# Optimization experiments

Measured on AMD Instinct MI355X. Metric: run time of the kernel, lower is better.

The kernel has to match this reference:

```python
import jax, jax.numpy as jnp
import numpy as np

N, E, B = 100000, 800000, 64
IN, HC1, HC2, NC, SA = 256, 128, 32, 2, 350
NEG = 0.2  # GATv2Conv default negative_slope


def forward(s_x, s_edge_index, s_batch, s_root_n_id,
            Wq, bq, Wk, bk, Wv, bv,
            Wl1, bl1, Wr1, br1, att1, bias1,
            Wl2, bl2, Wr2, br2, att2, bias2,
            Wl3, bl3, Wr3, br3, att3, bias3,
            c1w, c1b, c2W, c2b, c3W, c3b,
            linW, linb, aW1, ab1, aW2, mW1, mb1, mW2, mb2):
    src, dst = s_edge_index[0], s_edge_index[1]
    x_info = s_x
    # --- SelfAttention over seq_len=1 (x.unsqueeze(1)) ---
    z = s_x[:, None, :]                                   # [N,1,IN]
    q = z @ Wq + bq; k = z @ Wk + bk; v = z @ Wv + bv      # [N,1,SA]
    scores = jnp.einsum('nqd,nkd->nqk', q, k) / jnp.sqrt(jnp.float32(SA))
    probs = jax.nn.softmax(scores, axis=-1)
    h = jnp.einsum('nqk,nkd->nqd', probs, v)[:, 0, :]      # [N,SA]

    def gatv2(x, Wl, bl, Wr, br, att, bias):
        # PyG GATv2Conv, heads=1, eval mode (dropout off)
        xl = x @ Wl + bl                                   # source transform [N,O]
        xr = x @ Wr + br                                   # target transform [N,O]
        e = jax.nn.leaky_relu(xl[src] + xr[dst], NEG)      # [E,O]
        s = e @ att                                        # [E]
        smax = jax.ops.segment_max(s, dst, num_segments=N)
        smax = jnp.where(jnp.isfinite(smax), smax, 0.0)
        ex = jnp.exp(s - smax[dst])
        den = jax.ops.segment_sum(ex, dst, num_segments=N)
        alpha = ex / jnp.maximum(den[dst], 1e-16)
        return jax.ops.segment_sum(alpha[:, None] * xl[src], dst, num_segments=N) + bias

    h = jax.nn.relu(gatv2(h, Wl1, bl1, Wr1, br1, att1, bias1))
    h = jax.nn.relu(gatv2(h, Wl2, bl2, Wr2, br2, att2, bias2))
    h = jax.nn.relu(gatv2(h, Wl3, bl3, Wr3, br3, att3, bias3))   # [N,HC2]

    # --- readout: root node feature ++ global mean pool ---
    cnt = jax.ops.segment_sum(jnp.ones((N,), h.dtype), s_batch, num_segments=B)
    pooled = jax.ops.segment_sum(h, s_batch, num_segments=B) / jnp.maximum(cnt, 1.0)[:, None]
    sx = jnp.concatenate([h[s_root_n_id], pooled], axis=-1)       # [B,2*HC2]

    # --- info branch on raw root features ---
    info = x_info[s_root_n_id]                                    # [B,IN]
    info = c1w[0] * info[:, :-2] + c1w[1] * info[:, 1:-1] + c1w[2] * info[:, 2:] + c1b  # Conv1d(1,1,3)
    t = info.T                                                    # [IN-2,B]
    t = jax.nn.relu(c2W @ t + c2b[:, None])                       # [HC1,B]
    t = jax.nn.relu(c3W @ t + c3b[:, None])                       # [HC1//2,B]
    t = t.T                                                       # [B,HC1//2]
    L = t.shape[1]
    t = jax.nn.relu(t.reshape(B, HC2, L // HC2).mean(-1))         # AdaptiveAvgPool1d(HC2)

    sx = jax.nn.relu(sx @ linW + linb)                            # [B,HC2]

    # --- semantic attention over the two views ---
    emb = jnp.stack([sx, t], axis=1)                              # [B,2,HC2]
    w = jnp.tanh(emb @ aW1 + ab1) @ aW2                           # [B,2,1]
    beta = jax.nn.softmax(w, axis=1)
    emb = (beta * emb).sum(1)                                     # [B,HC2]

    return jax.nn.softmax(jnp.tanh(emb @ mW1 + mb1) @ mW2 + mb2, axis=1)  # [B,NC]


def setup_inputs() -> dict:
    keys = iter(jax.random.split(jax.random.key(0), 64))
    def nrm(*shape):
        return jax.random.normal(next(keys), shape, dtype=jnp.float32) * 0.05
    inp = {}
    inp['s_x'] = jax.random.normal(next(keys), (N, IN), dtype=jnp.float32)
    inp['s_edge_index'] = jax.random.randint(next(keys), (2, E), 0, N)
    inp['s_batch'] = jnp.sort(jax.random.randint(next(keys), (N,), 0, B))
    inp['s_root_n_id'] = jax.random.randint(next(keys), (B,), 0, N)
    inp['Wq'] = nrm(IN, SA); inp['bq'] = nrm(SA)
    inp['Wk'] = nrm(IN, SA); inp['bk'] = nrm(SA)
    inp['Wv'] = nrm(IN, SA); inp['bv'] = nrm(SA)
    inp['Wl1'] = nrm(SA, HC1); inp['bl1'] = nrm(HC1)
    inp['Wr1'] = nrm(SA, HC1); inp['br1'] = nrm(HC1)
    inp['att1'] = nrm(HC1); inp['bias1'] = nrm(HC1)
    inp['Wl2'] = nrm(HC1, HC1 // 2); inp['bl2'] = nrm(HC1 // 2)
    inp['Wr2'] = nrm(HC1, HC1 // 2); inp['br2'] = nrm(HC1 // 2)
    inp['att2'] = nrm(HC1 // 2); inp['bias2'] = nrm(HC1 // 2)
    inp['Wl3'] = nrm(HC1 // 2, HC2); inp['bl3'] = nrm(HC2)
    inp['Wr3'] = nrm(HC1 // 2, HC2); inp['br3'] = nrm(HC2)
    inp['att3'] = nrm(HC2); inp['bias3'] = nrm(HC2)
    inp['c1w'] = nrm(3); inp['c1b'] = nrm(1)
    inp['c2W'] = nrm(HC1, IN - 2); inp['c2b'] = nrm(HC1)
    inp['c3W'] = nrm(HC1 // 2, HC1); inp['c3b'] = nrm(HC1 // 2)
    inp['linW'] = nrm(2 * HC2, HC2); inp['linb'] = nrm(HC2)
    inp['aW1'] = nrm(HC2, 16); inp['ab1'] = nrm(16); inp['aW2'] = nrm(16, 1)
    inp['mW1'] = nrm(HC2, 16); inp['mb1'] = nrm(16)
    inp['mW2'] = nrm(16, NC); inp['mb2'] = nrm(NC)
    return inp


def reference(s_x, s_edge_index, s_batch, s_root_n_id,
              Wq, bq, Wk, bk, Wv, bv,
              Wl1, bl1, Wr1, br1, att1, bias1,
              Wl2, bl2, Wr2, br2, att2, bias2,
              Wl3, bl3, Wr3, br3, att3, bias3,
              c1w, c1b, c2W, c2b, c3W, c3b,
              linW, linb, aW1, ab1, aW2, mW1, mb1, mW2, mb2):
    return forward(s_x, s_edge_index, s_batch, s_root_n_id,
                   Wq, bq, Wk, bk, Wv, bv,
                   Wl1, bl1, Wr1, br1, att1, bias1,
                   Wl2, bl2, Wr2, br2, att2, bias2,
                   Wl3, bl3, Wr3, br3, att3, bias3,
                   c1w, c1b, c2W, c2b, c3W, c3b,
                   linW, linb, aW1, ab1, aW2, mW1, mb1, mW2, mb2)
```

## Files before the change

kernel.cpp:

```cpp
#include <hip/hip_runtime.h>
#include <hip/hip_bf16.h>
#include <math.h>

typedef unsigned short ushort_t;
typedef __attribute__((ext_vector_type(8))) short bfrag;
typedef __attribute__((ext_vector_type(4))) float ffrag;

constexpr int N_NODES = 100000;
constexpr int N_EDGES = 800000;
constexpr int NB      = 64;
constexpr int IN_F    = 256;
constexpr int HC1C    = 128;
constexpr int HC2C    = 32;
constexpr int SA_D    = 350;
constexpr float NEG   = 0.2f;

constexpr int SCAN_NBLK = (N_NODES + 255) / 256;
constexpr int MTILES    = (N_NODES + 63) / 64;

constexpr size_t OFF_WT1    = 0;
constexpr size_t OFF_WT2    = OFF_WT1 + 65536;
constexpr size_t OFF_WT3    = OFF_WT2 + 16384;
constexpr size_t OFF_BC1    = OFF_WT3 + 4096;
constexpr size_t OFF_BC2    = OFF_BC1 + 256;
constexpr size_t OFF_BC3    = OFF_BC2 + 128;
constexpr size_t OFF_XLR    = OFF_BC3 + 64;
constexpr size_t OFF_H      = OFF_XLR + (size_t)N_NODES * 256;
constexpr size_t OFF_DEG    = OFF_H + (size_t)N_NODES * 128;
constexpr size_t OFF_ROWPTR = OFF_DEG + N_NODES;
constexpr size_t OFF_CURSOR = OFF_ROWPTR + N_NODES + 1;
constexpr size_t OFF_BLKS   = OFF_CURSOR + N_NODES;
constexpr size_t OFF_BLKO   = OFF_BLKS + 512;
constexpr size_t OFF_CSRSRC = OFF_BLKO + 512;
constexpr size_t OFF_POOLED = OFF_CSRSRC + N_EDGES;
constexpr size_t OFF_CNT    = OFF_POOLED + NB * HC2C;
constexpr size_t OFF_SX     = OFF_CNT + NB;
constexpr size_t OFF_INFO   = OFF_SX + NB * HC2C;
constexpr size_t OFF_T1     = OFF_INFO + (size_t)NB * (IN_F - 2);
constexpr size_t OFF_T2     = OFF_T1 + (size_t)HC1C * NB;
constexpr size_t OFF_TT     = OFF_T2 + (size_t)NB * NB;
constexpr size_t WS_FLOATS  = OFF_TT + NB * HC2C;

__device__ __forceinline__ ushort_t f2bf(float f) {
  union { float f; unsigned int u; } a;
  a.f = f;
  unsigned int r = a.u + 0x7FFFu + ((a.u >> 16) & 1u);
  return (ushort_t)(r >> 16);
}
__device__ __forceinline__ float bf2f(ushort_t h) {
  union { unsigned int u; float f; } a;
  a.u = ((unsigned int)h) << 16;
  return a.f;
}

__global__ void k_wcomb(const float* __restrict__ Wv, const float* __restrict__ Wl1,
                        const float* __restrict__ Wr1, ushort_t* __restrict__ WT) {
  int t = blockIdx.x * blockDim.x + threadIdx.x;
  if (t >= 256 * 256) return;
  int n = t & 255;
  int k = t >> 8;
  const float* Wx = (n < 128) ? Wl1 : Wr1;
  int j = n & 127;
  float a = 0.f;
  for (int kk = 0; kk < SA_D; ++kk) a += Wv[k * SA_D + kk] * Wx[kk * 128 + j];
  ushort_t h = f2bf(a);
  WT[(size_t)n * 256 + k] = h;
  WT[65536 + (size_t)n * 256 + k] = f2bf(a - bf2f(h));
}

__global__ void k_bcomb(const float* __restrict__ bv, const float* __restrict__ Wl1,
                        const float* __restrict__ bl1, const float* __restrict__ Wr1,
                        const float* __restrict__ br1, float* __restrict__ bc) {
  int n = threadIdx.x;
  if (n >= 256) return;
  const float* Wx = (n < 128) ? Wl1 : Wr1;
  const float* bx = (n < 128) ? bl1 : br1;
  int j = n & 127;
  float a = bx[j];
  for (int kk = 0; kk < SA_D; ++kk) a += bv[kk] * Wx[kk * 128 + j];
  bc[n] = a;
}

template <int K, int C>
__global__ void k_wpack(const float* __restrict__ Wl, const float* __restrict__ bl,
                        const float* __restrict__ Wr, const float* __restrict__ br,
                        ushort_t* __restrict__ WT, float* __restrict__ bc) {
  constexpr int NN = 2 * C;
  int t = blockIdx.x * blockDim.x + threadIdx.x;
  if (t < NN) bc[t] = (t < C) ? bl[t] : br[t - C];
  if (t >= NN * K) return;
  int n = t % NN;
  int k = t / NN;
  float v = (n < C) ? Wl[k * C + n] : Wr[k * C + (n - C)];
  ushort_t h = f2bf(v);
  WT[(size_t)n * K + k] = h;
  WT[(size_t)NN * K + (size_t)n * K + k] = f2bf(v - bf2f(h));
}

__global__ void k_hist(const int* __restrict__ dst, int* __restrict__ deg) {
  int e = blockIdx.x * blockDim.x + threadIdx.x;
  if (e < N_EDGES) atomicAdd(deg + dst[e], 1);
}

__global__ void k_scan_local(const int* __restrict__ deg, int* __restrict__ row_ptr,
                             int* __restrict__ blk_sum) {
  __shared__ int sh[256];
  int t = threadIdx.x;
  int i = blockIdx.x * 256 + t;
  int v = (i < N_NODES) ? deg[i] : 0;
  sh[t] = v;
  __syncthreads();
  for (int off = 1; off < 256; off <<= 1) {
    int add = (t >= off) ? sh[t - off] : 0;
    __syncthreads();
    sh[t] += add;
    __syncthreads();
  }
  if (i < N_NODES) row_ptr[i] = sh[t] - v;
  if (t == 255) blk_sum[blockIdx.x] = sh[255];
}

__global__ void k_scan_blk(const int* __restrict__ blk_sum, int* __restrict__ blk_off) {
  __shared__ int sh[512];
  int t = threadIdx.x;
  int v = (t < SCAN_NBLK) ? blk_sum[t] : 0;
  sh[t] = v;
  __syncthreads();
  for (int off = 1; off < 512; off <<= 1) {
    int add = (t >= off) ? sh[t - off] : 0;
    __syncthreads();
    sh[t] += add;
    __syncthreads();
  }
  blk_off[t] = sh[t] - v;
}

__global__ void k_scan_add(int* __restrict__ row_ptr, const int* __restrict__ blk_off,
                           int* __restrict__ cursor) {
  int i = blockIdx.x * blockDim.x + threadIdx.x;
  if (i < N_NODES) {
    int v = row_ptr[i] + blk_off[i >> 8];
    row_ptr[i] = v;
    cursor[i] = v;
  }
  if (i == 0) row_ptr[N_NODES] = N_EDGES;
}

__global__ void k_fill(const int* __restrict__ src, const int* __restrict__ dst,
                       int* __restrict__ cursor, int* __restrict__ csr_src) {
  int e = blockIdx.x * blockDim.x + threadIdx.x;
  if (e >= N_EDGES) return;
  int pos = atomicAdd(cursor + dst[e], 1);
  csr_src[pos] = src[e];
}

template <int K, int NN, int BN>
__global__ __launch_bounds__(256) void k_gemm_mfma(const float* __restrict__ x,
                                                   const ushort_t* __restrict__ WT,
                                                   const float* __restrict__ bc,
                                                   float* __restrict__ out, int M) {
  constexpr int BM  = 64;
  constexpr int BK  = 32;
  constexpr int LDA = BK + 8;
  constexpr int NCT = BN / 16;
  __shared__ ushort_t As[2][BM * LDA];
  __shared__ ushort_t Bs[2][BN * LDA];
  const int tid  = threadIdx.x;
  const int wave = tid >> 6;
  const int lane = tid & 63;
  const int quad = lane >> 4;
  const int l16  = lane & 15;
  const int m0   = blockIdx.x * BM;
  const int n0   = blockIdx.y * BN;

  ffrag acc[NCT];
#pragma unroll
  for (int i = 0; i < NCT; ++i) acc[i] = ffrag{0.f, 0.f, 0.f, 0.f};

  for (int k0 = 0; k0 < K; k0 += BK) {
    __syncthreads();
    {
      int row = tid >> 2;
      int ks  = (tid & 3) * 8;
      int gm  = m0 + row;
      if (gm >= M) gm = M - 1;
      const float* srcp = x + (size_t)gm * K + k0 + ks;
      float4 v0 = ((const float4*)srcp)[0];
      float4 v1 = ((const float4*)srcp)[1];
      float v[8] = {v0.x, v0.y, v0.z, v0.w, v1.x, v1.y, v1.z, v1.w};
      ushort_t hi[8], lo[8];
#pragma unroll
      for (int j = 0; j < 8; ++j) {
        hi[j] = f2bf(v[j]);
        lo[j] = f2bf(v[j] - bf2f(hi[j]));
      }
      *(bfrag*)&As[0][row * LDA + ks] = *(const bfrag*)hi;
      *(bfrag*)&As[1][row * LDA + ks] = *(const bfrag*)lo;
    }
    for (int i = tid; i < BN * 4; i += 256) {
      int n  = i >> 2;
      int ks = (i & 3) * 8;
      const ushort_t* gh = WT + (size_t)(n0 + n) * K + k0 + ks;
      *(bfrag*)&Bs[0][n * LDA + ks] = *(const bfrag*)gh;
      *(bfrag*)&Bs[1][n * LDA + ks] = *(const bfrag*)(gh + (size_t)NN * K);
    }
    __syncthreads();

    bfrag a_hi = *(const bfrag*)&As[0][(wave * 16 + l16) * LDA + quad * 8];
    bfrag a_lo = *(const bfrag*)&As[1][(wave * 16 + l16) * LDA + quad * 8];
#pragma unroll
    for (int ct = 0; ct < NCT; ++ct) {
      bfrag b_hi = *(const bfrag*)&Bs[0][(ct * 16 + l16) * LDA + quad * 8];
      bfrag b_lo = *(const bfrag*)&Bs[1][(ct * 16 + l16) * LDA + quad * 8];
      acc[ct] = __builtin_amdgcn_mfma_f32_16x16x32_bf16(a_hi, b_hi, acc[ct], 0, 0, 0);
      acc[ct] = __builtin_amdgcn_mfma_f32_16x16x32_bf16(a_hi, b_lo, acc[ct], 0, 0, 0);
      acc[ct] = __builtin_amdgcn_mfma_f32_16x16x32_bf16(a_lo, b_hi, acc[ct], 0, 0, 0);
    }
  }

#pragma unroll
  for (int ct = 0; ct < NCT; ++ct) {
    int n = n0 + ct * 16 + l16;
    float b = bc[n];
#pragma unroll
    for (int r = 0; r < 4; ++r) {
      int m = m0 + wave * 16 + quad * 4 + r;
      if (m < M) out[(size_t)m * NN + n] = acc[ct][r] + b;
    }
  }
}

template <int C>
__global__ void k_gat(const float* __restrict__ xlr, const int* __restrict__ row_ptr,
                      const int* __restrict__ csr_src, const float* __restrict__ att,
                      const float* __restrict__ bias, float* __restrict__ h) {
  constexpr int G = C / 4;
  constexpr int RS = 2 * C;
  int t = blockIdx.x * blockDim.x + threadIdx.x;
  int d = t / G;
  int lane = t - d * G;
  if (d >= N_NODES) return;
  const float4 xr = *(const float4*)(xlr + (size_t)d * RS + C + lane * 4);
  const float4 a4 = *(const float4*)(att + lane * 4);
  float4 acc = {0.f, 0.f, 0.f, 0.f};
  float den = 0.f;
  const int e0 = row_ptr[d], e1 = row_ptr[d + 1];
  for (int i = e0; i < e1; ++i) {
    int s = csr_src[i];
    float4 xl = *(const float4*)(xlr + (size_t)s * RS + lane * 4);
    float v, p = 0.f;
    v = xl.x + xr.x; v = v > 0.f ? v : NEG * v; p += a4.x * v;
    v = xl.y + xr.y; v = v > 0.f ? v : NEG * v; p += a4.y * v;
    v = xl.z + xr.z; v = v > 0.f ? v : NEG * v; p += a4.z * v;
    v = xl.w + xr.w; v = v > 0.f ? v : NEG * v; p += a4.w * v;
#pragma unroll
    for (int off = G / 2; off > 0; off >>= 1) p += __shfl_xor(p, off, 64);
    float ex = expf(p);
    den += ex;
    acc.x += ex * xl.x;
    acc.y += ex * xl.y;
    acc.z += ex * xl.z;
    acc.w += ex * xl.w;
  }
  float inv = 1.f / fmaxf(den, 1e-16f);
  const float4 b4 = *(const float4*)(bias + lane * 4);
  float4 o;
  o.x = fmaxf(acc.x * inv + b4.x, 0.f);
  o.y = fmaxf(acc.y * inv + b4.y, 0.f);
  o.z = fmaxf(acc.z * inv + b4.z, 0.f);
  o.w = fmaxf(acc.w * inv + b4.w, 0.f);
  *(float4*)(h + (size_t)d * C + lane * 4) = o;
}

__global__ void k_pool(const float* __restrict__ h3, const int* __restrict__ batch,
                       float* __restrict__ pooled, float* __restrict__ cnt) {
  constexpr int NPB = 1024;
  constexpr int NPT = NPB / 8;
  int c = threadIdx.x & 31;
  int r = threadIdx.x >> 5;
  int base = blockIdx.x * NPB + r * NPT;
  if (base >= N_NODES) return;
  int end = base + NPT;
  if (end > N_NODES) end = N_NODES;
  int cur_b = batch[base];
  float acc = 0.f, count = 0.f;
  for (int n = base; n < end; ++n) {
    int b = batch[n];
    if (b != cur_b) {
      atomicAdd(pooled + cur_b * HC2C + c, acc);
      if (c == 0) atomicAdd(cnt + cur_b, count);
      cur_b = b;
      acc = 0.f;
      count = 0.f;
    }
    acc += h3[(size_t)n * HC2C + c];
    count += 1.f;
  }
  atomicAdd(pooled + cur_b * HC2C + c, acc);
  if (c == 0) atomicAdd(cnt + cur_b, count);
}

__global__ void k_sx(const float* __restrict__ h3, const int* __restrict__ root,
                     const float* __restrict__ pooled, const float* __restrict__ cnt,
                     const float* __restrict__ linW, const float* __restrict__ linb,
                     float* __restrict__ sx) {
  int t = blockIdx.x * blockDim.x + threadIdx.x;
  if (t >= NB * HC2C) return;
  int b = t >> 5, j = t & 31;
  int r = root[b];
  float inv = 1.f / fmaxf(cnt[b], 1.0f);
  float a = linb[j];
  for (int c = 0; c < HC2C; ++c) a += h3[(size_t)r * HC2C + c] * linW[c * HC2C + j];
  for (int c = 0; c < HC2C; ++c) a += (pooled[b * HC2C + c] * inv) * linW[(HC2C + c) * HC2C + j];
  sx[t] = a > 0.f ? a : 0.f;
}

__global__ void k_info1(const float* __restrict__ X, const int* __restrict__ root,
                        const float* __restrict__ c1w, const float* __restrict__ c1b,
                        float* __restrict__ info) {
  constexpr int L = IN_F - 2;
  int t = blockIdx.x * blockDim.x + threadIdx.x;
  if (t >= NB * L) return;
  int b = t / L, i = t - (t / L) * L;
  const float* xr = X + (size_t)root[b] * IN_F;
  info[t] = c1w[0] * xr[i] + c1w[1] * xr[i + 1] + c1w[2] * xr[i + 2] + c1b[0];
}

__global__ void k_info2(const float* __restrict__ info, const float* __restrict__ c2W,
                        const float* __restrict__ c2b, float* __restrict__ t1) {
  constexpr int L = IN_F - 2;
  int t = blockIdx.x * blockDim.x + threadIdx.x;
  if (t >= HC1C * NB) return;
  int j = t >> 6, b = t & 63;
  float a = c2b[j];
  for (int i = 0; i < L; ++i) a += c2W[j * L + i] * info[b * L + i];
  t1[t] = a > 0.f ? a : 0.f;
}

__global__ void k_info3(const float* __restrict__ t1, const float* __restrict__ c3W,
                        const float* __restrict__ c3b, float* __restrict__ t2) {
  int t = blockIdx.x * blockDim.x + threadIdx.x;
  if (t >= NB * NB) return;
  int j = t >> 6, b = t & 63;
  float a = c3b[j];
  for (int i = 0; i < HC1C; ++i) a += c3W[j * HC1C + i] * t1[i * NB + b];
  t2[t] = a > 0.f ? a : 0.f;
}

__global__ void k_info4(const float* __restrict__ t2, float* __restrict__ tt) {
  int t = blockIdx.x * blockDim.x + threadIdx.x;
  if (t >= NB * HC2C) return;
  int b = t >> 5, c = t & 31;
  float v = 0.5f * (t2[(2 * c) * NB + b] + t2[(2 * c + 1) * NB + b]);
  tt[b * HC2C + c] = v > 0.f ? v : 0.f;
}

__global__ void k_final(const float* __restrict__ sx, const float* __restrict__ tt,
                        const float* __restrict__ aW1, const float* __restrict__ ab1,
                        const float* __restrict__ aW2, const float* __restrict__ mW1,
                        const float* __restrict__ mb1, const float* __restrict__ mW2,
                        const float* __restrict__ mb2, float* __restrict__ out) {
  int b = threadIdx.x;
  if (b >= NB) return;
  const float* e0 = sx + b * HC2C;
  const float* e1 = tt + b * HC2C;
  float w[2];
#pragma unroll
  for (int r = 0; r < 2; ++r) {
    const float* eb = (r == 0) ? e0 : e1;
    float acc = 0.f;
    for (int j = 0; j < 16; ++j) {
      float z = ab1[j];
      for (int c = 0; c < HC2C; ++c) z += eb[c] * aW1[c * 16 + j];
      acc += tanhf(z) * aW2[j];
    }
    w[r] = acc;
  }
  float mx = fmaxf(w[0], w[1]);
  float x0 = expf(w[0] - mx), x1 = expf(w[1] - mx);
  float inv = 1.f / (x0 + x1);
  float b0 = x0 * inv, b1 = x1 * inv;
  float t16[16];
  for (int j = 0; j < 16; ++j) {
    float z = mb1[j];
    for (int c = 0; c < HC2C; ++c) z += (b0 * e0[c] + b1 * e1[c]) * mW1[c * 16 + j];
    t16[j] = tanhf(z);
  }
  float l0 = mb2[0], l1 = mb2[1];
  for (int j = 0; j < 16; ++j) {
    l0 += t16[j] * mW2[j * 2 + 0];
    l1 += t16[j] * mW2[j * 2 + 1];
  }
  float m2 = fmaxf(l0, l1);
  float y0 = expf(l0 - m2), y1 = expf(l1 - m2);
  float is = 1.f / (y0 + y1);
  out[b * 2 + 0] = y0 * is;
  out[b * 2 + 1] = y1 * is;
}

extern "C" void kernel_launch(void* const* d_in, const int* in_sizes, int n_in, void* d_out,
                              int out_size, void* d_ws, size_t ws_size, hipStream_t stream) {
  if (ws_size < WS_FLOATS * sizeof(float)) return;

  const float* s_x   = (const float*)d_in[0];
  const int*   edge  = (const int*)d_in[1];
  const int*   batch = (const int*)d_in[2];
  const int*   root  = (const int*)d_in[3];
  const float* Wv    = (const float*)d_in[8];
  const float* bv    = (const float*)d_in[9];
  const float* Wl1   = (const float*)d_in[10];
  const float* bl1   = (const float*)d_in[11];
  const float* Wr1   = (const float*)d_in[12];
  const float* br1   = (const float*)d_in[13];
  const float* att1  = (const float*)d_in[14];
  const float* bias1 = (const float*)d_in[15];
  const float* Wl2   = (const float*)d_in[16];
  const float* bl2   = (const float*)d_in[17];
  const float* Wr2   = (const float*)d_in[18];
  const float* br2   = (const float*)d_in[19];
  const float* att2  = (const float*)d_in[20];
  const float* bias2 = (const float*)d_in[21];
  const float* Wl3   = (const float*)d_in[22];
  const float* bl3   = (const float*)d_in[23];
  const float* Wr3   = (const float*)d_in[24];
  const float* br3   = (const float*)d_in[25];
  const float* att3  = (const float*)d_in[26];
  const float* bias3 = (const float*)d_in[27];
  const float* c1w   = (const float*)d_in[28];
  const float* c1b   = (const float*)d_in[29];
  const float* c2W   = (const float*)d_in[30];
  const float* c2b   = (const float*)d_in[31];
  const float* c3W   = (const float*)d_in[32];
  const float* c3b   = (const float*)d_in[33];
  const float* linW  = (const float*)d_in[34];
  const float* linb  = (const float*)d_in[35];
  const float* aW1   = (const float*)d_in[36];
  const float* ab1   = (const float*)d_in[37];
  const float* aW2   = (const float*)d_in[38];
  const float* mW1   = (const float*)d_in[39];
  const float* mb1   = (const float*)d_in[40];
  const float* mW2   = (const float*)d_in[41];
  const float* mb2   = (const float*)d_in[42];

  const int* src = edge;
  const int* dst = edge + N_EDGES;

  float*    ws      = (float*)d_ws;
  ushort_t* WT1     = (ushort_t*)(ws + OFF_WT1);
  ushort_t* WT2     = (ushort_t*)(ws + OFF_WT2);
  ushort_t* WT3     = (ushort_t*)(ws + OFF_WT3);
  float*    bc1     = ws + OFF_BC1;
  float*    bc2     = ws + OFF_BC2;
  float*    bc3     = ws + OFF_BC3;
  float*    xlr     = ws + OFF_XLR;
  float*    hbuf    = ws + OFF_H;
  int*      deg     = (int*)(ws + OFF_DEG);
  int*      row_ptr = (int*)(ws + OFF_ROWPTR);
  int*      cursor  = (int*)(ws + OFF_CURSOR);
  int*      blks    = (int*)(ws + OFF_BLKS);
  int*      blko    = (int*)(ws + OFF_BLKO);
  int*      csr_src = (int*)(ws + OFF_CSRSRC);
  float*    pooled  = ws + OFF_POOLED;
  float*    cnt     = ws + OFF_CNT;
  float*    sx      = ws + OFF_SX;
  float*    info    = ws + OFF_INFO;
  float*    t1      = ws + OFF_T1;
  float*    t2      = ws + OFF_T2;
  float*    tt      = ws + OFF_TT;
  float*    out     = (float*)d_out;

  hipMemsetAsync(deg, 0, N_NODES * sizeof(int), stream);
  k_hist<<<(N_EDGES + 255) / 256, 256, 0, stream>>>(dst, deg);
  k_scan_local<<<SCAN_NBLK, 256, 0, stream>>>(deg, row_ptr, blks);
  k_scan_blk<<<1, 512, 0, stream>>>(blks, blko);
  k_scan_add<<<SCAN_NBLK, 256, 0, stream>>>(row_ptr, blko, cursor);
  k_fill<<<(N_EDGES + 255) / 256, 256, 0, stream>>>(src, dst, cursor, csr_src);

  k_wcomb<<<(256 * 256) / 256, 256, 0, stream>>>(Wv, Wl1, Wr1, WT1);
  k_bcomb<<<1, 256, 0, stream>>>(bv, Wl1, bl1, Wr1, br1, bc1);
  k_wpack<128, 64><<<(128 * 128 + 255) / 256, 256, 0, stream>>>(Wl2, bl2, Wr2, br2, WT2, bc2);
  k_wpack<64, 32><<<(64 * 64 + 255) / 256, 256, 0, stream>>>(Wl3, bl3, Wr3, br3, WT3, bc3);

  k_gemm_mfma<256, 256, 128><<<dim3(MTILES, 2), 256, 0, stream>>>(s_x, WT1, bc1, xlr, N_NODES);
  k_gat<128><<<(N_NODES * 32 + 255) / 256, 256, 0, stream>>>(xlr, row_ptr, csr_src, att1,
                                                             bias1, hbuf);

  k_gemm_mfma<128, 128, 128><<<dim3(MTILES, 1), 256, 0, stream>>>(hbuf, WT2, bc2, xlr, N_NODES);
  k_gat<64><<<(N_NODES * 16 + 255) / 256, 256, 0, stream>>>(xlr, row_ptr, csr_src, att2,
                                                            bias2, hbuf);

  k_gemm_mfma<64, 64, 64><<<dim3(MTILES, 1), 256, 0, stream>>>(hbuf, WT3, bc3, xlr, N_NODES);
  k_gat<32><<<(N_NODES * 8 + 255) / 256, 256, 0, stream>>>(xlr, row_ptr, csr_src, att3,
                                                           bias3, hbuf);

  hipMemsetAsync(pooled, 0, (NB * HC2C + NB) * sizeof(float), stream);
  k_pool<<<(N_NODES + 1023) / 1024, 256, 0, stream>>>(hbuf, batch, pooled, cnt);
  k_sx<<<(NB * HC2C + 255) / 256, 256, 0, stream>>>(hbuf, root, pooled, cnt, linW, linb, sx);

  k_info1<<<(NB * (IN_F - 2) + 255) / 256, 256, 0, stream>>>(s_x, root, c1w, c1b, info);
  k_info2<<<(HC1C * NB + 255) / 256, 256, 0, stream>>>(info, c2W, c2b, t1);
  k_info3<<<(NB * NB + 255) / 256, 256, 0, stream>>>(t1, c3W, c3b, t2);
  k_info4<<<(NB * HC2C + 255) / 256, 256, 0, stream>>>(t2, tt);

  k_final<<<1, NB, 0, stream>>>(sx, tt, aW1, ab1, aW2, mW1, mb1, mW2, mb2, out);
}
```

Measured before the change: 723.8 us.

## Enlarge GEMM tile to 128 rows and full N, cheaper bf16 split

The split-bf16 MFMA GEMM now covers 128 rows per block (two 16-row subtiles per wave) and the full output width, so the first layer's A tile is loaded and split once instead of once per N-half. The hi/lo bf16 split switches from round-to-nearest to truncation using byte-permute packing, which cuts ALU work. The trade-offs are more accumulator registers and fewer blocks (about 782), so occupancy may drop. Truncating the hi part leaves a larger lo residual, but the 3-product scheme still gives close to fp32 accuracy.

```diff
diff --git a/kernel.cpp b/kernel.cpp
--- a/kernel.cpp
+++ b/kernel.cpp
@@ -16,7 +16,7 @@
 constexpr float NEG   = 0.2f;
 
 constexpr int SCAN_NBLK = (N_NODES + 255) / 256;
-constexpr int MTILES    = (N_NODES + 63) / 64;
+constexpr int MB128     = (N_NODES + 127) / 128;
 
 constexpr size_t OFF_WT1    = 0;
 constexpr size_t OFF_WT2    = OFF_WT1 + 65536;
@@ -52,6 +52,13 @@
   a.u = ((unsigned int)h) << 16;
   return a.f;
 }
+__device__ __forceinline__ void split2(float a, float b, unsigned int& hi, unsigned int& lo) {
+  unsigned int ua = __float_as_uint(a), ub = __float_as_uint(b);
+  float la = a - __uint_as_float(ua & 0xFFFF0000u);
+  float lb = b - __uint_as_float(ub & 0xFFFF0000u);
+  hi = __builtin_amdgcn_perm(ub, ua, 0x07060302u);
+  lo = __builtin_amdgcn_perm(__float_as_uint(lb), __float_as_uint(la), 0x07060302u);
+}
 
 __global__ void k_wcomb(const float* __restrict__ Wv, const float* __restrict__ Wl1,
                         const float* __restrict__ Wr1, ushort_t* __restrict__ WT) {
@@ -154,80 +161,95 @@
   csr_src[pos] = src[e];
 }
 
-template <int K, int NN, int BN>
+template <int K, int NN>
 __global__ __launch_bounds__(256) void k_gemm_mfma(const float* __restrict__ x,
                                                    const ushort_t* __restrict__ WT,
                                                    const float* __restrict__ bc,
                                                    float* __restrict__ out, int M) {
-  constexpr int BM  = 64;
+  constexpr int BM  = 128;
   constexpr int BK  = 32;
   constexpr int LDA = BK + 8;
-  constexpr int NCT = BN / 16;
+  constexpr int NCT = NN / 16;
   __shared__ ushort_t As[2][BM * LDA];
-  __shared__ ushort_t Bs[2][BN * LDA];
+  __shared__ ushort_t Bs[2][NN * LDA];
   const int tid  = threadIdx.x;
   const int wave = tid >> 6;
   const int lane = tid & 63;
   const int quad = lane >> 4;
   const int l16  = lane & 15;
   const int m0   = blockIdx.x * BM;
-  const int n0   = blockIdx.y * BN;
-
-  ffrag acc[NCT];
-#pragma unroll
-  for (int i = 0; i < NCT; ++i) acc[i] = ffrag{0.f, 0.f, 0.f, 0.f};
+
+  ffrag acc[2][NCT];
+#pragma unroll
+  for (int rt = 0; rt < 2; ++rt)
+#pragma unroll
+    for (int i = 0; i < NCT; ++i) acc[rt][i] = ffrag{0.f, 0.f, 0.f, 0.f};
 
   for (int k0 = 0; k0 < K; k0 += BK) {
     __syncthreads();
     {
-      int row = tid >> 2;
-      int ks  = (tid & 3) * 8;
+      int row = tid >> 1;
+      int ks  = (tid & 1) * 16;
       int gm  = m0 + row;
       if (gm >= M) gm = M - 1;
-      const float* srcp = x + (size_t)gm * K + k0 + ks;
-      float4 v0 = ((const float4*)srcp)[0];
-      float4 v1 = ((const float4*)srcp)[1];
-      float v[8] = {v0.x, v0.y, v0.z, v0.w, v1.x, v1.y, v1.z, v1.w};
-      ushort_t hi[8], lo[8];
-#pragma unroll
-      for (int j = 0; j < 8; ++j) {
-        hi[j] = f2bf(v[j]);
-        lo[j] = f2bf(v[j] - bf2f(hi[j]));
-      }
-      *(bfrag*)&As[0][row * LDA + ks] = *(const bfrag*)hi;
-      *(bfrag*)&As[1][row * LDA + ks] = *(const bfrag*)lo;
-    }
-    for (int i = tid; i < BN * 4; i += 256) {
+      const float4* sp = (const float4*)(x + (size_t)gm * K + k0 + ks);
+      float4 f0 = sp[0], f1 = sp[1], f2 = sp[2], f3 = sp[3];
+      unsigned int hi[8], lo[8];
+      split2(f0.x, f0.y, hi[0], lo[0]);
+      split2(f0.z, f0.w, hi[1], lo[1]);
+      split2(f1.x, f1.y, hi[2], lo[2]);
+      split2(f1.z, f1.w, hi[3], lo[3]);
+      split2(f2.x, f2.y, hi[4], lo[4]);
+      split2(f2.z, f2.w, hi[5], lo[5]);
+      split2(f3.x, f3.y, hi[6], lo[6]);
+      split2(f3.z, f3.w, hi[7], lo[7]);
+      *(uint4*)&As[0][row * LDA + ks]     = *(uint4*)&hi[0];
+      *(uint4*)&As[0][row * LDA + ks + 8] = *(uint4*)&hi[4];
+      *(uint4*)&As[1][row * LDA + ks]     = *(uint4*)&lo[0];
+      *(uint4*)&As[1][row * LDA + ks + 8] = *(uint4*)&lo[4];
+    }
+#pragma unroll
+    for (int i = tid; i < NN * 4; i += 256) {
       int n  = i >> 2;
       int ks = (i & 3) * 8;
-      const ushort_t* gh = WT + (size_t)(n0 + n) * K + k0 + ks;
+      const ushort_t* gh = WT + (size_t)n * K + k0 + ks;
       *(bfrag*)&Bs[0][n * LDA + ks] = *(const bfrag*)gh;
       *(bfrag*)&Bs[1][n * LDA + ks] = *(const bfrag*)(gh + (size_t)NN * K);
     }
     __syncthreads();
 
-    bfrag a_hi = *(const bfrag*)&As[0][(wave * 16 + l16) * LDA + quad * 8];
-    bfrag a_lo = *(const bfrag*)&As[1][(wave * 16 + l16) * LDA + quad * 8];
+    bfrag a_hi[2], a_lo[2];
+#pragma unroll
+    for (int rt = 0; rt < 2; ++rt) {
+      int r = wave * 32 + rt * 16 + l16;
+      a_hi[rt] = *(const bfrag*)&As[0][r * LDA + quad * 8];
+      a_lo[rt] = *(const bfrag*)&As[1][r * LDA + quad * 8];
+    }
 #pragma unroll
     for (int ct = 0; ct < NCT; ++ct) {
       bfrag b_hi = *(const bfrag*)&Bs[0][(ct * 16 + l16) * LDA + quad * 8];
       bfrag b_lo = *(const bfrag*)&Bs[1][(ct * 16 + l16) * LDA + quad * 8];
-      acc[ct] = __builtin_amdgcn_mfma_f32_16x16x32_bf16(a_hi, b_hi, acc[ct], 0, 0, 0);
-      acc[ct] = __builtin_amdgcn_mfma_f32_16x16x32_bf16(a_hi, b_lo, acc[ct], 0, 0, 0);
-      acc[ct] = __builtin_amdgcn_mfma_f32_16x16x32_bf16(a_lo, b_hi, acc[ct], 0, 0, 0);
-    }
-  }
-
-#pragma unroll
-  for (int ct = 0; ct < NCT; ++ct) {
-    int n = n0 + ct * 16 + l16;
-    float b = bc[n];
-#pragma unroll
-    for (int r = 0; r < 4; ++r) {
-      int m = m0 + wave * 16 + quad * 4 + r;
-      if (m < M) out[(size_t)m * NN + n] = acc[ct][r] + b;
-    }
-  }
+#pragma unroll
+      for (int rt = 0; rt < 2; ++rt) {
+        acc[rt][ct] = __builtin_amdgcn_mfma_f32_16x16x32_bf16(a_hi[rt], b_hi, acc[rt][ct], 0, 0, 0);
+        acc[rt][ct] = __builtin_amdgcn_mfma_f32_16x16x32_bf16(a_hi[rt], b_lo, acc[rt][ct], 0, 0, 0);
+        acc[rt][ct] = __builtin_amdgcn_mfma_f32_16x16x32_bf16(a_lo[rt], b_hi, acc[rt][ct], 0, 0, 0);
+      }
+    }
+  }
+
+#pragma unroll
+  for (int rt = 0; rt < 2; ++rt)
+#pragma unroll
+    for (int ct = 0; ct < NCT; ++ct) {
+      int n = ct * 16 + l16;
+      float b = bc[n];
+#pragma unroll
+      for (int r = 0; r < 4; ++r) {
+        int m = m0 + wave * 32 + rt * 16 + quad * 4 + r;
+        if (m < M) out[(size_t)m * NN + n] = acc[rt][ct][r] + b;
+      }
+    }
 }
 
 template <int C>
@@ -481,15 +503,15 @@
   k_wpack<128, 64><<<(128 * 128 + 255) / 256, 256, 0, stream>>>(Wl2, bl2, Wr2, br2, WT2, bc2);
   k_wpack<64, 32><<<(64 * 64 + 255) / 256, 256, 0, stream>>>(Wl3, bl3, Wr3, br3, WT3, bc3);
 
-  k_gemm_mfma<256, 256, 128><<<dim3(MTILES, 2), 256, 0, stream>>>(s_x, WT1, bc1, xlr, N_NODES);
+  k_gemm_mfma<256, 256><<<MB128, 256, 0, stream>>>(s_x, WT1, bc1, xlr, N_NODES);
   k_gat<128><<<(N_NODES * 32 + 255) / 256, 256, 0, stream>>>(xlr, row_ptr, csr_src, att1,
                                                              bias1, hbuf);
 
-  k_gemm_mfma<128, 128, 128><<<dim3(MTILES, 1), 256, 0, stream>>>(hbuf, WT2, bc2, xlr, N_NODES);
+  k_gemm_mfma<128, 128><<<MB128, 256, 0, stream>>>(hbuf, WT2, bc2, xlr, N_NODES);
   k_gat<64><<<(N_NODES * 16 + 255) / 256, 256, 0, stream>>>(xlr, row_ptr, csr_src, att2,
                                                             bias2, hbuf);
 
-  k_gemm_mfma<64, 64, 64><<<dim3(MTILES, 1), 256, 0, stream>>>(hbuf, WT3, bc3, xlr, N_NODES);
+  k_gemm_mfma<64, 64><<<MB128, 256, 0, stream>>>(hbuf, WT3, bc3, xlr, N_NODES);
   k_gat<32><<<(N_NODES * 8 + 255) / 256, 256, 0, stream>>>(xlr, row_ptr, csr_src, att3,
                                                            bias3, hbuf);
 
```

New measurement: 794.2 us. +9.7%, slower.
